# Kernel optimization log

Measured on AMD Instinct MI355X. Metric: run time of the kernel, lower is better.

## Reference

```python
import jax, jax.numpy as jnp
import numpy as np

T_HORIZON = 1.0
REG = 0.01


def setup_inputs() -> dict:
    key = jax.random.key(0)
    kx, = jax.random.split(key, 1)
    B, N = 2, 8192
    # sorted event times in [0, 1); horizon T = 1.0 > all events
    x = jnp.sort(jax.random.uniform(kx, (B, N), dtype=jnp.float32), axis=-1)
    mu = jnp.full((1,), 0.5, dtype=jnp.float32)
    alpha = jnp.full((1,), 0.5, dtype=jnp.float32)
    w = jnp.full((1,), 1.0, dtype=jnp.float32)
    return {"x": x, "mu": mu, "alpha": alpha, "w": w}


def reference(x, mu, alpha, w):
    # x: [B, N] event times; mu/alpha/w: shape (1,) Hawkes parameters
    # delta[b, i, j] = x[b, j] - x[b, i]
    delta = x[:, None, :] - x[:, :, None]                       # [B, N, N]
    # masked_fill(delta <= 0, -inf) then exp -> exactly zero on non-causal pairs
    kern = jnp.exp(-w * jnp.where(delta > 0, delta, jnp.inf))   # [B, N, N]
    # sum over dim=1 (i.e. over past events i for each event j)
    excite = alpha * w * jnp.sum(kern, axis=1)                  # [B, N]
    pos = jnp.log(mu + excite)                                  # [B, N]
    neg = alpha * (1.0 - jnp.exp(-w * (T_HORIZON - x)))         # [B, N]
    nll = mu * T_HORIZON - jnp.sum(pos) + jnp.sum(neg)          # shape (1,)
    loss = nll + REG * (-jnp.log(mu) - jnp.log(alpha) - jnp.log(w))
    return loss
```

## Files before the change

kernel.cpp:

```cpp
#include <hip/hip_runtime.h>
#include <math.h>


#define BLOCK 1024
#define ITEMS 8
#define NWAVES (BLOCK / 64)

__launch_bounds__(BLOCK)
__global__ void hawkes_nll_kernel(const float* __restrict__ x,
                                  const float* __restrict__ mu_p,
                                  const float* __restrict__ alpha_p,
                                  const float* __restrict__ w_p,
                                  float* __restrict__ out,
                                  int B) {
    const float mu    = mu_p[0];
    const float alpha = alpha_p[0];
    const float w     = w_p[0];
    const float aw    = alpha * w;

    const int tid  = threadIdx.x;
    const int lane = tid & 63;
    const int wave = tid >> 6;

    __shared__ float  s_wave[NWAVES];
    __shared__ double s_pos[NWAVES];
    __shared__ double s_neg[NWAVES];

    double pos_sum = 0.0;
    double neg_sum = 0.0;

    const int N = BLOCK * ITEMS;

    for (int b = 0; b < B; ++b) {
        const float* xb = x + (size_t)b * N;
        const int base = tid * ITEMS;

        float xs[ITEMS];
        float ys[ITEMS];
        float tsum = 0.0f;
#pragma unroll
        for (int i = 0; i < ITEMS; ++i) {
            xs[i] = xb[base + i];
            ys[i] = __expf(w * xs[i]);
            tsum += ys[i];
        }

        float v = tsum;
#pragma unroll
        for (int off = 1; off < 64; off <<= 1) {
            float n = __shfl_up(v, off, 64);
            if (lane >= off) v += n;
        }
        if (lane == 63) s_wave[wave] = v;
        __syncthreads();
        if (wave == 0) {
            float t = (lane < NWAVES) ? s_wave[lane] : 0.0f;
#pragma unroll
            for (int off = 1; off < NWAVES; off <<= 1) {
                float n = __shfl_up(t, off, 64);
                if (lane >= off) t += n;
            }
            if (lane < NWAVES) s_wave[lane] = t;
        }
        __syncthreads();
        float run = ((wave == 0) ? 0.0f : s_wave[wave - 1]) + (v - tsum);

#pragma unroll
        for (int i = 0; i < ITEMS; ++i) {
            float S = __expf(-w * xs[i]) * run;
            pos_sum += (double)__logf(mu + aw * S);
            neg_sum += (double)(alpha * (1.0f - __expf(-w * (1.0f - xs[i]))));
            run += ys[i];
        }
        __syncthreads();
    }

#pragma unroll
    for (int off = 32; off > 0; off >>= 1) {
        pos_sum += __shfl_down(pos_sum, off, 64);
        neg_sum += __shfl_down(neg_sum, off, 64);
    }
    if (lane == 0) { s_pos[wave] = pos_sum; s_neg[wave] = neg_sum; }
    __syncthreads();
    if (tid == 0) {
        double P = 0.0, Ng = 0.0;
#pragma unroll
        for (int i = 0; i < NWAVES; ++i) { P += s_pos[i]; Ng += s_neg[i]; }
        const double T_HORIZON = 1.0;
        const double REG = 0.01;
        double nll = (double)mu * T_HORIZON - P + Ng;
        double loss = nll + REG * (-log((double)mu) - log((double)alpha) - log((double)w));
        out[0] = (float)loss;
    }
}

extern "C" void kernel_launch(void* const* d_in, const int* in_sizes, int n_in,
                              void* d_out, int out_size, void* d_ws, size_t ws_size,
                              hipStream_t stream) {
    const float* x     = (const float*)d_in[0];
    const float* mu    = (const float*)d_in[1];
    const float* alpha = (const float*)d_in[2];
    const float* w     = (const float*)d_in[3];
    float* out = (float*)d_out;

    const int N = BLOCK * ITEMS;
    const int B = in_sizes[0] / N;

    hipLaunchKernelGGL(hawkes_nll_kernel, dim3(1), dim3(BLOCK), 0, stream,
                       x, mu, alpha, w, out, B);
}
```

Before: 63.88 us.

## Split scan across many blocks with redundant prefix sums and atomic reduction

Replaces the single-block sequential loop over batches with B*16 blocks, each handling one 512-element chunk of a row. Each block recomputes the exp-prefix of all earlier elements in its row with vectorised loads, then scans its own chunk, and combines its partial loss into the output with an atomic add after a memset. It also replaces the per-element exp(-w*x) with a reciprocal of the cached exp(w*x) and folds the neg term algebraically into alpha - alpha*exp(-w)*exp(w*x). The cost is redundant prefix work that grows with chunk index, an extra memset launch, and a different float summation order.

```diff
diff --git a/kernel.cpp b/kernel.cpp
--- a/kernel.cpp
+++ b/kernel.cpp
@@ -2,77 +2,89 @@
 #include <math.h>
 
 
-#define BLOCK 1024
-#define ITEMS 8
-#define NWAVES (BLOCK / 64)
+#define BLOCK   256
+#define CHUNKS  16
+#define NROW    8192
+#define M       (NROW / CHUNKS)
+#define ITEMS   (M / BLOCK)
+#define NWAVES  (BLOCK / 64)
 
 __launch_bounds__(BLOCK)
 __global__ void hawkes_nll_kernel(const float* __restrict__ x,
                                   const float* __restrict__ mu_p,
                                   const float* __restrict__ alpha_p,
                                   const float* __restrict__ w_p,
-                                  float* __restrict__ out,
-                                  int B) {
+                                  float* __restrict__ out) {
     const float mu    = mu_p[0];
     const float alpha = alpha_p[0];
     const float w     = w_p[0];
     const float aw    = alpha * w;
+    const float cneg  = alpha * __expf(-w);
 
     const int tid  = threadIdx.x;
     const int lane = tid & 63;
     const int wave = tid >> 6;
 
-    __shared__ float  s_wave[NWAVES];
+    const int b = blockIdx.x / CHUNKS;
+    const int c = blockIdx.x % CHUNKS;
+
+    const float* xb = x + (size_t)b * NROW;
+
+    __shared__ float  s_pre[NWAVES];
+    __shared__ float  s_scan[NWAVES];
     __shared__ double s_pos[NWAVES];
     __shared__ double s_neg[NWAVES];
 
-    double pos_sum = 0.0;
-    double neg_sum = 0.0;
+    float esum = 0.0f;
+    {
+        const float4* x4 = (const float4*)xb;
+        const int npre4 = (c * M) >> 2;
+        for (int i = tid; i < npre4; i += BLOCK) {
+            float4 v = x4[i];
+            esum += __expf(w * v.x) + __expf(w * v.y)
+                  + __expf(w * v.z) + __expf(w * v.w);
+        }
+#pragma unroll
+        for (int off = 32; off > 0; off >>= 1)
+            esum += __shfl_down(esum, off, 64);
+        if (lane == 0) s_pre[wave] = esum;
+    }
 
-    const int N = BLOCK * ITEMS;
+    const int base = c * M + tid * ITEMS;
+    float xs[ITEMS], ys[ITEMS];
+    float tsum = 0.0f;
+#pragma unroll
+    for (int i = 0; i < ITEMS; ++i) {
+        xs[i] = xb[base + i];
+        ys[i] = __expf(w * xs[i]);
+        tsum += ys[i];
+    }
 
-    for (int b = 0; b < B; ++b) {
-        const float* xb = x + (size_t)b * N;
-        const int base = tid * ITEMS;
+    float v = tsum;
+#pragma unroll
+    for (int off = 1; off < 64; off <<= 1) {
+        float n = __shfl_up(v, off, 64);
+        if (lane >= off) v += n;
+    }
+    if (lane == 63) s_scan[wave] = v;
+    __syncthreads();
 
-        float xs[ITEMS];
-        float ys[ITEMS];
-        float tsum = 0.0f;
+    float E = 0.0f;
 #pragma unroll
-        for (int i = 0; i < ITEMS; ++i) {
-            xs[i] = xb[base + i];
-            ys[i] = __expf(w * xs[i]);
-            tsum += ys[i];
-        }
+    for (int i = 0; i < NWAVES; ++i) E += s_pre[i];
+    float wavepre = 0.0f;
+#pragma unroll
+    for (int i = 0; i < NWAVES; ++i) if (i < wave) wavepre += s_scan[i];
 
-        float v = tsum;
+    float run = E + wavepre + (v - tsum);
+
+    double pos_sum = 0.0, neg_sum = 0.0;
 #pragma unroll
-        for (int off = 1; off < 64; off <<= 1) {
-            float n = __shfl_up(v, off, 64);
-            if (lane >= off) v += n;
-        }
-        if (lane == 63) s_wave[wave] = v;
-        __syncthreads();
-        if (wave == 0) {
-            float t = (lane < NWAVES) ? s_wave[lane] : 0.0f;
-#pragma unroll
-            for (int off = 1; off < NWAVES; off <<= 1) {
-                float n = __shfl_up(t, off, 64);
-                if (lane >= off) t += n;
-            }
-            if (lane < NWAVES) s_wave[lane] = t;
-        }
-        __syncthreads();
-        float run = ((wave == 0) ? 0.0f : s_wave[wave - 1]) + (v - tsum);
-
-#pragma unroll
-        for (int i = 0; i < ITEMS; ++i) {
-            float S = __expf(-w * xs[i]) * run;
-            pos_sum += (double)__logf(mu + aw * S);
-            neg_sum += (double)(alpha * (1.0f - __expf(-w * (1.0f - xs[i]))));
-            run += ys[i];
-        }
-        __syncthreads();
+    for (int i = 0; i < ITEMS; ++i) {
+        float S = run * __builtin_amdgcn_rcpf(ys[i]);
+        pos_sum += (double)__logf(mu + aw * S);
+        neg_sum += (double)(alpha - cneg * ys[i]);
+        run += ys[i];
     }
 
 #pragma unroll
@@ -86,11 +98,15 @@
         double P = 0.0, Ng = 0.0;
 #pragma unroll
         for (int i = 0; i < NWAVES; ++i) { P += s_pos[i]; Ng += s_neg[i]; }
-        const double T_HORIZON = 1.0;
-        const double REG = 0.01;
-        double nll = (double)mu * T_HORIZON - P + Ng;
-        double loss = nll + REG * (-log((double)mu) - log((double)alpha) - log((double)w));
-        out[0] = (float)loss;
+        float partial = (float)(Ng - P);
+        if (blockIdx.x == 0) {
+            const double T_HORIZON = 1.0;
+            const double REG = 0.01;
+            partial += (float)((double)mu * T_HORIZON
+                     + REG * (-log((double)mu) - log((double)alpha)
+                              - log((double)w)));
+        }
+        atomicAdd(out, partial);
     }
 }
 
@@ -103,9 +119,9 @@
     const float* w     = (const float*)d_in[3];
     float* out = (float*)d_out;
 
-    const int N = BLOCK * ITEMS;
-    const int B = in_sizes[0] / N;
+    const int B = in_sizes[0] / NROW;
 
-    hipLaunchKernelGGL(hawkes_nll_kernel, dim3(1), dim3(BLOCK), 0, stream,
-                       x, mu, alpha, w, out, B);
+    hipMemsetAsync(out, 0, sizeof(float), stream);
+    hipLaunchKernelGGL(hawkes_nll_kernel, dim3(B * CHUNKS), dim3(BLOCK), 0, stream,
+                       x, mu, alpha, w, out);
 }
```

After: 62.96 us. Within noise of the previous version (-1.4%).
